# Kernel tuning notes

Measured on AMD Instinct MI355X. Metric: run time of the kernel, lower is better.

Reference implementation:

```python
import jax, jax.numpy as jnp
import numpy as np

CH = 512   # ch_in = c_out
P = 8
SD = 512
NG = CH // P          # n_groups = 64
CIG = CH // NG        # c_in per group = 8
DN = ('NCHW', 'OIHW', 'NCHW')


def setup_inputs() -> dict:
    key = jax.random.key(0)
    ks = jax.random.split(key, 8)
    N, H, W = 8, 128, 128
    return {
        "style_encoding": jax.random.normal(ks[0], (N, SD, 4, 4), jnp.float32),
        "predicted": jax.random.normal(ks[1], (N, CH, H, W), jnp.float32),
        "dw_w": jax.random.normal(ks[2], (CH * CIG, SD, 2, 2), jnp.float32) * 0.02,
        "dw_b": jnp.zeros((CH * CIG,), jnp.float32),
        "pk_w": jax.random.normal(ks[3], (CH * CIG, SD), jnp.float32) * 0.02,
        "pk_b": jnp.zeros((CH * CIG,), jnp.float32),
        "pb_w": jax.random.normal(ks[4], (CH, SD), jnp.float32) * 0.02,
        "pb_b": jnp.zeros((CH,), jnp.float32),
    }


def reference(style_encoding, predicted, dw_w, dw_b, pk_w, pk_b, pb_w, pb_b):
    N, ch, h, w = predicted.shape
    # --- KernelPredictor ---
    # depthwise kernels: 2x2 conv on 4x4 style -> 3x3 spatial kernels
    dw = jax.lax.conv_general_dilated(style_encoding, dw_w, (1, 1), 'VALID',
                                      dimension_numbers=DN)
    dw = dw + dw_b[None, :, None, None]
    depthwise = dw.reshape(N, CH, CIG, 3, 3)
    # avg-pool 4x4 -> (N, SD); 1x1 convs become matmuls
    s_pool = style_encoding.mean(axis=(2, 3))
    pw_kn = (s_pool @ pk_w.T + pk_b).reshape(N, CH, CH // NG)
    pw_bias = s_pool @ pb_w.T + pb_b  # (N, CH)
    # --- instance norm (calc_mean_std, unbiased var, eps=1e-5) ---
    mean = predicted.mean(axis=(2, 3), keepdims=True)
    std = jnp.sqrt(predicted.var(axis=(2, 3), keepdims=True, ddof=1) + 1e-5)
    x = (predicted - mean) / std
    # --- reflect pad + per-sample grouped convs, batched as groups ---
    x = jnp.pad(x, ((0, 0), (0, 0), (1, 1), (1, 1)), mode='reflect')
    xb = x.reshape(1, N * ch, h + 2, w + 2)
    wb = depthwise.reshape(N * CH, CIG, 3, 3)
    depth = jax.lax.conv_general_dilated(xb, wb, (1, 1), 'VALID',
                                         dimension_numbers=DN,
                                         feature_group_count=N * NG)
    wp = pw_kn.reshape(N * CH, CH // NG, 1, 1)
    out = jax.lax.conv_general_dilated(depth, wp, (1, 1), 'VALID',
                                       dimension_numbers=DN,
                                       feature_group_count=N * NG)
    out = out + pw_bias.reshape(1, N * CH, 1, 1)
    return out.reshape(N, ch, h, w)
```

## Files before the change

### kernel.cpp

```cpp
#include <hip/hip_runtime.h>

#define N_    8
#define CH_   512
#define SD_   512
#define CIG_  8
#define NG_   64
#define H_    128
#define W_    128
#define HW_   16384
#define KDW   2048
#define NP_   72
#define OC_   4096

#define WS_B     0
#define WS_SPOOL (WS_B + NP_ * KDW)
#define WS_PWKN  (WS_SPOOL + N_ * SD_)
#define WS_PWB   (WS_PWKN + N_ * OC_)
#define WS_DW    (WS_PWB + N_ * CH_)
#define WS_E     (WS_DW + N_ * OC_ * 9)
#define WS_MEAN  (WS_E + N_ * OC_ * 9)
#define WS_RSTD  (WS_MEAN + N_ * CH_)

#define NZERO (N_ * OC_ + N_ * CH_ + N_ * OC_ * 9)

__global__ __launch_bounds__(256) void prep(const float* __restrict__ style,
                                            float* __restrict__ B,
                                            float* __restrict__ spool,
                                            float* __restrict__ zbase) {
  const int idx = blockIdx.x * 256 + threadIdx.x;
  const int NB = NP_ * KDW;
  const int NS = N_ * SD_;
  if (idx < NB) {
    const int np = idx >> 11;
    const int k = idx & 2047;
    const int n = np / 9, p = np % 9;
    const int py = p / 3, px = p % 3;
    const int ci = k >> 2, uv = k & 3;
    const int u = uv >> 1, v = uv & 1;
    B[idx] = style[(n * SD_ + ci) * 16 + (py + u) * 4 + (px + v)];
  } else if (idx < NB + NS) {
    const int j = idx - NB;
    const float* s = style + j * 16;
    float a = 0.f;
#pragma unroll
    for (int t = 0; t < 16; t++) a += s[t];
    spool[j] = a * (1.0f / 16.0f);
  } else if (idx < NB + NS + NZERO) {
    zbase[idx - NB - NS] = 0.0f;
  }
}

__global__ __launch_bounds__(256) void stats(const float* __restrict__ pred,
                                             float* __restrict__ meanv,
                                             float* __restrict__ rstdv) {
  const int nc = blockIdx.x;
  const float4* p = (const float4*)(pred + (size_t)nc * HW_);
  float s = 0.f, s2 = 0.f;
#pragma unroll
  for (int i = 0; i < 16; i++) {
    const float4 v = p[threadIdx.x + 256 * i];
    s += v.x + v.y + v.z + v.w;
    s2 += v.x * v.x + v.y * v.y + v.z * v.z + v.w * v.w;
  }
  for (int off = 32; off > 0; off >>= 1) {
    s += __shfl_down(s, off, 64);
    s2 += __shfl_down(s2, off, 64);
  }
  __shared__ float as[4], as2[4];
  const int wv = threadIdx.x >> 6;
  if ((threadIdx.x & 63) == 0) { as[wv] = s; as2[wv] = s2; }
  __syncthreads();
  if (threadIdx.x == 0) {
    const float S = as[0] + as[1] + as[2] + as[3];
    const float S2 = as2[0] + as2[1] + as2[2] + as2[3];
    const float mean = S * (1.0f / HW_);
    const float var = (S2 - S * mean) * (1.0f / (HW_ - 1));
    meanv[nc] = mean;
    rstdv[nc] = 1.0f / sqrtf(var + 1e-5f);
  }
}

__global__ __launch_bounds__(256) void pw_gemm(const float* __restrict__ spool,
                                               const float* __restrict__ pkw,
                                               const float* __restrict__ pkb,
                                               const float* __restrict__ pbw,
                                               const float* __restrict__ pbb,
                                               float* __restrict__ pwkn,
                                               float* __restrict__ pwbias) {
  __shared__ float sp[N_ * 128];
  const int kb = blockIdx.y * 128;
  for (int i = threadIdx.x; i < N_ * 128; i += 256) {
    const int nn = i >> 7, kk = i & 127;
    sp[i] = spool[nn * SD_ + kb + kk];
  }
  __syncthreads();
  const int col = blockIdx.x * 256 + threadIdx.x;
  const float* w;
  float bias;
  if (col < OC_) { w = pkw + (size_t)col * SD_ + kb; bias = pkb[col]; }
  else           { w = pbw + (size_t)(col - OC_) * SD_ + kb; bias = pbb[col - OC_]; }
  float acc[8];
#pragma unroll
  for (int nn = 0; nn < 8; nn++) acc[nn] = 0.f;
  for (int k = 0; k < 128; k += 4) {
    const float4 wv = *(const float4*)(w + k);
#pragma unroll
    for (int nn = 0; nn < 8; nn++) {
      const float4 sv = *(const float4*)(&sp[nn * 128 + k]);
      acc[nn] = fmaf(wv.x, sv.x, acc[nn]);
      acc[nn] = fmaf(wv.y, sv.y, acc[nn]);
      acc[nn] = fmaf(wv.z, sv.z, acc[nn]);
      acc[nn] = fmaf(wv.w, sv.w, acc[nn]);
    }
  }
  const float badd = (blockIdx.y == 0) ? bias : 0.0f;
  if (col < OC_) {
#pragma unroll
    for (int nn = 0; nn < 8; nn++)
      atomicAdd(&pwkn[nn * OC_ + col], acc[nn] + badd);
  } else {
#pragma unroll
    for (int nn = 0; nn < 8; nn++)
      atomicAdd(&pwbias[nn * CH_ + (col - OC_)], acc[nn] + badd);
  }
}

__global__ __launch_bounds__(256) void dw_gemm(const float* __restrict__ Bg,
                                               const float* __restrict__ Wg,
                                               float* __restrict__ dwacc) {
  __shared__ float Wl[64 * 129];
  const int t = threadIdx.x;
  const int co0 = blockIdx.x * 128;
  const int kbase = blockIdx.y * 128;
  const int co = t & 127;
  const int npb = __builtin_amdgcn_readfirstlane((t >> 7) * 36);
  float acc[36];
#pragma unroll
  for (int j = 0; j < 36; j++) acc[j] = 0.f;

  for (int kc = 0; kc < 128; kc += 64) {
    __syncthreads();
    {
      const int kq = (t & 15) * 4;
      const int cob = t >> 4;
#pragma unroll
      for (int r = 0; r < 8; r++) {
        const int c = cob + r * 16;
        const float4 wv =
            *(const float4*)(Wg + (size_t)(co0 + c) * KDW + kbase + kc + kq);
        Wl[(kq + 0) * 129 + c] = wv.x;
        Wl[(kq + 1) * 129 + c] = wv.y;
        Wl[(kq + 2) * 129 + c] = wv.z;
        Wl[(kq + 3) * 129 + c] = wv.w;
      }
    }
    __syncthreads();
    const float* Bp = Bg + kbase + kc;
    for (int k = 0; k < 64; k += 4) {
      const float w0 = Wl[(k + 0) * 129 + co];
      const float w1 = Wl[(k + 1) * 129 + co];
      const float w2 = Wl[(k + 2) * 129 + co];
      const float w3 = Wl[(k + 3) * 129 + co];
#pragma unroll
      for (int j = 0; j < 36; j++) {
        const float4 b = *(const float4*)(Bp + (npb + j) * KDW + k);
        float a = acc[j];
        a = fmaf(w0, b.x, a);
        a = fmaf(w1, b.y, a);
        a = fmaf(w2, b.z, a);
        a = fmaf(w3, b.w, a);
        acc[j] = a;
      }
    }
  }
#pragma unroll
  for (int j = 0; j < 36; j++) {
    const int np = npb + j;
    const int n = np / 9, p = np % 9;
    atomicAdd(dwacc + (size_t)(n * OC_ + co0 + co) * 9 + p, acc[j]);
  }
}

__global__ __launch_bounds__(256) void eff_k(const float* __restrict__ dwacc,
                                             const float* __restrict__ dwb,
                                             const float* __restrict__ pwkn,
                                             float* __restrict__ Eg) {
  const int idx = blockIdx.x * 256 + threadIdx.x;
  const int co = idx & 7;
  int tmp = idx >> 3;
  const int p = tmp % 9;
  tmp /= 9;
  const int ci = tmp & 7;
  tmp >>= 3;
  const int gc = tmp & 63;
  const int n = tmp >> 6;
  const int c = gc * 8 + co;
  float a = 0.f;
#pragma unroll
  for (int j = 0; j < 8; j++) {
    const int ch = (gc * 8 + j) * 8 + ci;
    a = fmaf(pwkn[n * OC_ + c * 8 + j],
             dwacc[(size_t)(n * OC_ + ch) * 9 + p] + dwb[ch], a);
  }
  Eg[idx] = a;
}

#define ROWS 16
__global__ __launch_bounds__(256, 4) void main_conv(
    const float* __restrict__ pred, const float* __restrict__ Eg,
    const float* __restrict__ pwb, const float* __restrict__ meanv,
    const float* __restrict__ rstdv, float* __restrict__ out) {
  __shared__ float xl[4 * 18 * 132];
  __shared__ float El[8 * 9 * 8];
  __shared__ float cm[8], cr[8];
  const int t = threadIdx.x;
  const int yt = blockIdx.x;
  const int gc = blockIdx.y;
  const int n = blockIdx.z;
  const int chbase = n * CH_ + gc * 8;

  if (t < 8) {
    cm[t] = meanv[chbase + t];
    cr[t] = rstdv[chbase + t];
  }
  for (int i = t; i < 576; i += 256)
    El[i] = Eg[(size_t)(n * 64 + gc) * 576 + i];
  __syncthreads();

  const int y0 = yt * ROWS;
  const int y = t >> 4;
  const int xb = (t & 15) * 8;
  float acc[8][8];
#pragma unroll
  for (int co = 0; co < 8; co++)
#pragma unroll
    for (int px = 0; px < 8; px++) acc[co][px] = 0.f;

#pragma unroll 1
  for (int half = 0; half < 2; half++) {
    if (half) __syncthreads();
    for (int i = t; i < 4 * 18 * 130; i += 256) {
      const int col = i % 130;
      const int rr = (i / 130) % 18;
      const int cl = i / (130 * 18);
      const int ci = half * 4 + cl;
      int gy = y0 + rr - 1;
      gy = gy < 0 ? -gy : (gy > 127 ? 254 - gy : gy);
      int gx = col - 1;
      gx = gx < 0 ? -gx : (gx > 127 ? 254 - gx : gx);
      const float v = pred[((size_t)(chbase + ci) * 128 + gy) * 128 + gx];
      xl[(cl * 18 + rr) * 132 + col] = (v - cm[ci]) * cr[ci];
    }
    __syncthreads();

#pragma unroll 1
    for (int cl = 0; cl < 4; cl++) {
      const int ci = half * 4 + cl;
#pragma unroll
      for (int ky = 0; ky < 3; ky++) {
        const float* xr = &xl[(cl * 18 + y + ky) * 132 + xb];
        const float4 xa = *(const float4*)(xr);
        const float4 xc = *(const float4*)(xr + 4);
        const float xw[10] = {xa.x, xa.y, xa.z, xa.w, xc.x,
                              xc.y, xc.z, xc.w, xr[8], xr[9]};
#pragma unroll
        for (int kx = 0; kx < 3; kx++) {
          const float4 e0 = *(const float4*)(&El[(ci * 9 + ky * 3 + kx) * 8]);
          const float4 e1 =
              *(const float4*)(&El[(ci * 9 + ky * 3 + kx) * 8 + 4]);
          const float ev[8] = {e0.x, e0.y, e0.z, e0.w,
                               e1.x, e1.y, e1.z, e1.w};
#pragma unroll
          for (int co = 0; co < 8; co++)
#pragma unroll
            for (int px = 0; px < 8; px++)
              acc[co][px] = fmaf(ev[co], xw[kx + px], acc[co][px]);
        }
      }
    }
  }

  const int gy = y0 + y;
#pragma unroll
  for (int co = 0; co < 8; co++) {
    const float b = pwb[chbase + co];
    float* op = out + ((size_t)(chbase + co) * 128 + gy) * 128 + xb;
    float4 o0, o1;
    o0.x = acc[co][0] + b; o0.y = acc[co][1] + b;
    o0.z = acc[co][2] + b; o0.w = acc[co][3] + b;
    o1.x = acc[co][4] + b; o1.y = acc[co][5] + b;
    o1.z = acc[co][6] + b; o1.w = acc[co][7] + b;
    *(float4*)op = o0;
    *(float4*)(op + 4) = o1;
  }
}

extern "C" void kernel_launch(void* const* d_in, const int* in_sizes, int n_in,
                              void* d_out, int out_size, void* d_ws,
                              size_t ws_size, hipStream_t stream) {
  const float* style = (const float*)d_in[0];
  const float* pred = (const float*)d_in[1];
  const float* dww = (const float*)d_in[2];
  const float* dwb = (const float*)d_in[3];
  const float* pkw = (const float*)d_in[4];
  const float* pkb = (const float*)d_in[5];
  const float* pbw = (const float*)d_in[6];
  const float* pbb = (const float*)d_in[7];
  float* out = (float*)d_out;
  float* ws = (float*)d_ws;

  float* B = ws + WS_B;
  float* spool = ws + WS_SPOOL;
  float* pwkn = ws + WS_PWKN;
  float* pwbias = ws + WS_PWB;
  float* dwacc = ws + WS_DW;
  float* Eg = ws + WS_E;
  float* meanv = ws + WS_MEAN;
  float* rstdv = ws + WS_RSTD;

  prep<<<dim3(1888), dim3(256), 0, stream>>>(style, B, spool, pwkn);
  stats<<<dim3(4096), dim3(256), 0, stream>>>(pred, meanv, rstdv);
  pw_gemm<<<dim3(18, 4), dim3(256), 0, stream>>>(spool, pkw, pkb, pbw, pbb,
                                                 pwkn, pwbias);
  dw_gemm<<<dim3(32, 16), dim3(256), 0, stream>>>(B, dww, dwacc);
  eff_k<<<dim3(1152), dim3(256), 0, stream>>>(dwacc, dwb, pwkn, Eg);
  main_conv<<<dim3(8, 64, 8), dim3(256), 0, stream>>>(pred, Eg, pwbias, meanv,
                                                      rstdv, out);
}
```

Before: 957.3 us.

## Fold instance-norm into conv weights and bias, retile main conv

The per-channel rstd scale is folded into the effective 3x3 weights, and the mean term is subtracted from the output bias with atomic adds in eff_k. This lets main_conv load raw input with float4 vector loads and skip per-element normalization. Reflect padding on the left and right is now handled by choosing edge indices in registers. The main conv tile shrinks to 8 rows, with each thread computing 4 output channels instead of 8, which doubles the grid, cuts registers and shared memory, and drops the occupancy hint. The atomic bias accumulation relies on pwbias already being written by pw_gemm, which runs earlier, and changes the order of floating-point summation.

```diff
diff --git a/kernel.cpp b/kernel.cpp
--- a/kernel.cpp
+++ b/kernel.cpp
@@ -184,7 +184,10 @@
 __global__ __launch_bounds__(256) void eff_k(const float* __restrict__ dwacc,
                                              const float* __restrict__ dwb,
                                              const float* __restrict__ pwkn,
-                                             float* __restrict__ Eg) {
+                                             const float* __restrict__ meanv,
+                                             const float* __restrict__ rstdv,
+                                             float* __restrict__ Eg,
+                                             float* __restrict__ pwbias) {
   const int idx = blockIdx.x * 256 + threadIdx.x;
   const int co = idx & 7;
   int tmp = idx >> 3;
@@ -202,89 +205,91 @@
     a = fmaf(pwkn[n * OC_ + c * 8 + j],
              dwacc[(size_t)(n * OC_ + ch) * 9 + p] + dwb[ch], a);
   }
-  Eg[idx] = a;
-}
-
-#define ROWS 16
-__global__ __launch_bounds__(256, 4) void main_conv(
+  const int cin = n * CH_ + gc * 8 + ci;
+  const float ep = a * rstdv[cin];
+  Eg[idx] = ep;
+  atomicAdd(&pwbias[n * CH_ + c], -ep * meanv[cin]);
+}
+
+#define ROWS 8
+__global__ __launch_bounds__(256) void main_conv(
     const float* __restrict__ pred, const float* __restrict__ Eg,
-    const float* __restrict__ pwb, const float* __restrict__ meanv,
-    const float* __restrict__ rstdv, float* __restrict__ out) {
-  __shared__ float xl[4 * 18 * 132];
-  __shared__ float El[8 * 9 * 8];
-  __shared__ float cm[8], cr[8];
+    const float* __restrict__ pwb, float* __restrict__ out) {
+  __shared__ float xl[4 * 10 * 132];
+  __shared__ float Elh[288];
   const int t = threadIdx.x;
   const int yt = blockIdx.x;
   const int gc = blockIdx.y;
   const int n = blockIdx.z;
   const int chbase = n * CH_ + gc * 8;
-
-  if (t < 8) {
-    cm[t] = meanv[chbase + t];
-    cr[t] = rstdv[chbase + t];
-  }
-  for (int i = t; i < 576; i += 256)
-    El[i] = Eg[(size_t)(n * 64 + gc) * 576 + i];
-  __syncthreads();
-
   const int y0 = yt * ROWS;
-  const int y = t >> 4;
+
+  const int y = t >> 5;
+  const int ch4 = ((t >> 4) & 1) * 4;
   const int xb = (t & 15) * 8;
-  float acc[8][8];
-#pragma unroll
-  for (int co = 0; co < 8; co++)
+  const int li = (xb == 0) ? 1 : xb - 1;
+  const int ri = (xb == 120) ? 126 : xb + 8;
+
+  float acc[4][8];
+#pragma unroll
+  for (int co = 0; co < 4; co++)
 #pragma unroll
     for (int px = 0; px < 8; px++) acc[co][px] = 0.f;
 
+  const float* egb = Eg + (size_t)(n * 64 + gc) * 576;
+
 #pragma unroll 1
-  for (int half = 0; half < 2; half++) {
-    if (half) __syncthreads();
-    for (int i = t; i < 4 * 18 * 130; i += 256) {
-      const int col = i % 130;
-      const int rr = (i / 130) % 18;
-      const int cl = i / (130 * 18);
-      const int ci = half * 4 + cl;
+  for (int h = 0; h < 2; h++) {
+    if (h) __syncthreads();
+    for (int i = t; i < 1280; i += 256) {
+      const int ci_l = (i >> 6) / 5;
+      const int r = i - ci_l * 320;
+      const int rr = r >> 5;
+      const int q = r & 31;
       int gy = y0 + rr - 1;
-      gy = gy < 0 ? -gy : (gy > 127 ? 254 - gy : gy);
-      int gx = col - 1;
-      gx = gx < 0 ? -gx : (gx > 127 ? 254 - gx : gx);
-      const float v = pred[((size_t)(chbase + ci) * 128 + gy) * 128 + gx];
-      xl[(cl * 18 + rr) * 132 + col] = (v - cm[ci]) * cr[ci];
-    }
+      gy = gy < 0 ? 1 : (gy > 127 ? 126 : gy);
+      const float4 v = *(const float4*)(
+          pred + (((size_t)(chbase + h * 4 + ci_l) << 7) + gy) * 128 +
+          (q << 2));
+      *(float4*)(&xl[(ci_l * 10 + rr) * 132 + (q << 2)]) = v;
+    }
+    for (int i = t; i < 288; i += 256) Elh[i] = egb[h * 288 + i];
     __syncthreads();
 
 #pragma unroll 1
     for (int cl = 0; cl < 4; cl++) {
-      const int ci = half * 4 + cl;
+      const float* xbase = xl + cl * 1320;
 #pragma unroll
       for (int ky = 0; ky < 3; ky++) {
-        const float* xr = &xl[(cl * 18 + y + ky) * 132 + xb];
-        const float4 xa = *(const float4*)(xr);
-        const float4 xc = *(const float4*)(xr + 4);
-        const float xw[10] = {xa.x, xa.y, xa.z, xa.w, xc.x,
-                              xc.y, xc.z, xc.w, xr[8], xr[9]};
+        const float* xrow = xbase + (y + ky) * 132;
+        const float4 xa = *(const float4*)(xrow + xb);
+        const float4 xc = *(const float4*)(xrow + xb + 4);
+        float xw[10];
+        xw[0] = xrow[li];
+        xw[1] = xa.x; xw[2] = xa.y; xw[3] = xa.z; xw[4] = xa.w;
+        xw[5] = xc.x; xw[6] = xc.y; xw[7] = xc.z; xw[8] = xc.w;
+        xw[9] = xrow[ri];
 #pragma unroll
         for (int kx = 0; kx < 3; kx++) {
-          const float4 e0 = *(const float4*)(&El[(ci * 9 + ky * 3 + kx) * 8]);
-          const float4 e1 =
-              *(const float4*)(&El[(ci * 9 + ky * 3 + kx) * 8 + 4]);
-          const float ev[8] = {e0.x, e0.y, e0.z, e0.w,
-                               e1.x, e1.y, e1.z, e1.w};
-#pragma unroll
-          for (int co = 0; co < 8; co++)
+          const float4 e =
+              *(const float4*)(&Elh[(cl * 9 + ky * 3 + kx) * 8 + ch4]);
+          const float ev[4] = {e.x, e.y, e.z, e.w};
+#pragma unroll
+          for (int co = 0; co < 4; co++)
 #pragma unroll
             for (int px = 0; px < 8; px++)
-              acc[co][px] = fmaf(ev[co], xw[kx + px], acc[co][px]);
+              acc[co][px] = fmaf(ev[co], xw[px + kx], acc[co][px]);
         }
       }
     }
   }
 
-  const int gy = y0 + y;
-#pragma unroll
-  for (int co = 0; co < 8; co++) {
-    const float b = pwb[chbase + co];
-    float* op = out + ((size_t)(chbase + co) * 128 + gy) * 128 + xb;
+  const int gyo = y0 + y;
+#pragma unroll
+  for (int co = 0; co < 4; co++) {
+    const int c = chbase + ch4 + co;
+    const float b = pwb[c];
+    float* op = out + ((size_t)c * 128 + gyo) * 128 + xb;
     float4 o0, o1;
     o0.x = acc[co][0] + b; o0.y = acc[co][1] + b;
     o0.z = acc[co][2] + b; o0.w = acc[co][3] + b;
@@ -323,7 +328,7 @@
   pw_gemm<<<dim3(18, 4), dim3(256), 0, stream>>>(spool, pkw, pkb, pbw, pbb,
                                                  pwkn, pwbias);
   dw_gemm<<<dim3(32, 16), dim3(256), 0, stream>>>(B, dww, dwacc);
-  eff_k<<<dim3(1152), dim3(256), 0, stream>>>(dwacc, dwb, pwkn, Eg);
-  main_conv<<<dim3(8, 64, 8), dim3(256), 0, stream>>>(pred, Eg, pwbias, meanv,
-                                                      rstdv, out);
-}
+  eff_k<<<dim3(1152), dim3(256), 0, stream>>>(dwacc, dwb, pwkn, meanv, rstdv,
+                                              Eg, pwbias);
+  main_conv<<<dim3(16, 64, 8), dim3(256), 0, stream>>>(pred, Eg, pwbias, out);
+}
```

After: 815.4 us. 14.8% less time.
